# Optimization experiments

Measured on AMD Instinct MI355X. Metric: run time of the kernel, lower is better.

The kernel has to match this reference:

```python
import jax, jax.numpy as jnp
import numpy as np

N_NODES = 100000
N_EDGES = 3200000
D = 256
REPEAT = 2
FACTOR = 0.5


def setup_inputs() -> dict:
    key = jax.random.key(0)
    k1, k2, k3, k4, k5, k6 = jax.random.split(key, 6)
    x = jax.random.normal(k1, (N_NODES, D), dtype=jnp.float32)
    vals = jax.random.uniform(k2, (N_EDGES,), dtype=jnp.float32)
    # Xavier-ish scale for linear weights
    W0 = jax.random.normal(k3, (D, D), dtype=jnp.float32) / np.sqrt(D)
    W1 = jax.random.normal(k4, (D, D), dtype=jnp.float32) / np.sqrt(D)
    rows = jax.random.randint(k5, (N_EDGES,), 0, N_NODES, dtype=jnp.int32)
    cols = jax.random.randint(k6, (N_EDGES,), 0, N_NODES, dtype=jnp.int32)
    return {"x": x, "vals": vals, "W0": W0, "W1": W1, "rows": rows, "cols": cols}


def reference(x, vals, W0, W1, rows, cols):
    # support is sparse [N, N] in COO: support[rows[e], cols[e]] = vals[e]
    def spmm(h):
        # gather source-node features, scale by edge weight, scatter-add to dst
        return jax.ops.segment_sum(vals[:, None] * h[cols], rows,
                                   num_segments=N_NODES)

    h = x
    for W, act in ((W0, jax.nn.relu), (W1, lambda v: v)):
        # _propagate: repeated SpMM with scalar factor
        for _ in range(REPEAT):
            h = spmm(h) * FACTOR
        # linear (no bias) + activation
        h = act(h @ W)
    return h
```

## Files before the change

### kernel.cpp

```cpp
#include <hip/hip_runtime.h>
#include <hip/hip_bf16.h>
#include <hip/hip_fp16.h>

#define N_D 256
#define NBLK 832

typedef __attribute__((ext_vector_type(8))) short bf16x8;
typedef __attribute__((ext_vector_type(4))) float f32x4;

__device__ __forceinline__ unsigned short f2bf(float f) {
  union { float f; unsigned u; } c; c.f = f;
  unsigned u = c.u;
  return (unsigned short)((u + 0x7fffu + ((u >> 16) & 1u)) >> 16);
}
__device__ __forceinline__ float asf(unsigned u) {
  union { unsigned u; float f; } c; c.u = u;
  return c.f;
}
__device__ __forceinline__ int grp_of(int r, unsigned gmagic) {
  int g = (int)(((unsigned long long)(unsigned)r * gmagic) >> 37);
  return min(g, 7);
}

__global__ __launch_bounds__(256) void conv_kernel(
    const float* __restrict__ in, unsigned short* __restrict__ out, int n4) {
  int i = blockIdx.x * 256 + threadIdx.x;
  if (i < n4) {
    float4 v = reinterpret_cast<const float4*>(in)[i];
    ushort4 o;
    o.x = f2bf(v.x); o.y = f2bf(v.y); o.z = f2bf(v.z); o.w = f2bf(v.w);
    reinterpret_cast<ushort4*>(out)[i] = o;
  }
}

__global__ __launch_bounds__(256) void count_kernel(
    const int* __restrict__ rows, int* __restrict__ cnt8, int* __restrict__ cntT,
    int n_edges, unsigned gmagic, int M) {
  __shared__ int lcnt[8];
  if (threadIdx.x < 8) lcnt[threadIdx.x] = 0;
  __syncthreads();
  int* __restrict__ cnt = cnt8 + (size_t)(blockIdx.x & 7) * M;
  for (int e = blockIdx.x * 256 + threadIdx.x; e < n_edges; e += NBLK * 256) {
    const int r = rows[e];
    atomicAdd(&cnt[r], 1);
    atomicAdd(&lcnt[grp_of(r, gmagic)], 1);
  }
  __syncthreads();
  if (threadIdx.x < 8) cntT[threadIdx.x * NBLK + blockIdx.x] = lcnt[threadIdx.x];
}

__global__ __launch_bounds__(256) void sumcnt_kernel(
    const int* __restrict__ cnt8, int* __restrict__ cnts,
    int* __restrict__ bsum, int M) {
  __shared__ int wred[4];
  const int i = blockIdx.x * 256 + threadIdx.x;
  int s = 0;
  if (i < M) {
#pragma unroll
    for (int k = 0; k < 8; ++k) s += cnt8[(size_t)k * M + i];
    cnts[i] = s;
  }
  int t = s;
#pragma unroll
  for (int off = 32; off; off >>= 1) t += __shfl_down(t, off, 64);
  if ((threadIdx.x & 63) == 0) wred[threadIdx.x >> 6] = t;
  __syncthreads();
  if (threadIdx.x == 0) bsum[blockIdx.x] = wred[0] + wred[1] + wred[2] + wred[3];
}

__global__ __launch_bounds__(1024) void scan_kernel(
    const int* __restrict__ cnt, int* __restrict__ outA,
    int* __restrict__ outB, int n) {
  __shared__ int wsum[16];
  __shared__ int carry_sh;
  const int tid = threadIdx.x;
  const int lane = tid & 63;
  const int wid = tid >> 6;
  if (tid == 0) carry_sh = 0;
  __syncthreads();
  for (int base = 0; base < n; base += 4096) {
    const int i0 = base + tid * 4;
    int4 v = make_int4(0, 0, 0, 0);
    if (i0 + 3 < n) v = *reinterpret_cast<const int4*>(cnt + i0);
    else {
      if (i0     < n) v.x = cnt[i0];
      if (i0 + 1 < n) v.y = cnt[i0 + 1];
      if (i0 + 2 < n) v.z = cnt[i0 + 2];
    }
    const int s1 = v.x, s2 = s1 + v.y, s3 = s2 + v.z, s4 = s3 + v.w;
    int ws = s4;
#pragma unroll
    for (int off = 1; off < 64; off <<= 1) {
      int o = __shfl_up(ws, off, 64);
      if (lane >= off) ws += o;
    }
    if (lane == 63) wsum[wid] = ws;
    __syncthreads();
    if (wid == 0) {
      int t = (lane < 16) ? wsum[lane] : 0;
#pragma unroll
      for (int off = 1; off < 16; off <<= 1) {
        int o = __shfl_up(t, off, 64);
        if (lane >= off) t += o;
      }
      if (lane < 16) wsum[lane] = t;
    }
    __syncthreads();
    const int carry = carry_sh;
    const int tbase = carry + (wid ? wsum[wid - 1] : 0) + ws - s4;
    if (i0     < n) { outA[i0]     = tbase;      outB[i0]     = tbase; }
    if (i0 + 1 < n) { outA[i0 + 1] = tbase + s1; outB[i0 + 1] = tbase + s1; }
    if (i0 + 2 < n) { outA[i0 + 2] = tbase + s2; outB[i0 + 2] = tbase + s2; }
    if (i0 + 3 < n) { outA[i0 + 3] = tbase + s3; outB[i0 + 3] = tbase + s3; }
    __syncthreads();
    if (tid == 0) carry_sh = carry + wsum[15];
    __syncthreads();
  }
  if (tid == 0) outA[n] = carry_sh;
}

__global__ __launch_bounds__(256) void scan_apply_kernel(
    const int* __restrict__ cnts, const int* __restrict__ bofs,
    int* __restrict__ row_ptr, int* __restrict__ cursor, int M) {
  __shared__ int wsum[4];
  const int tid = threadIdx.x;
  const int lane = tid & 63;
  const int wid = tid >> 6;
  const int i = blockIdx.x * 256 + tid;
  const int v = (i < M) ? cnts[i] : 0;
  int s = v;
#pragma unroll
  for (int off = 1; off < 64; off <<= 1) {
    int o = __shfl_up(s, off, 64);
    if (lane >= off) s += o;
  }
  if (lane == 63) wsum[wid] = s;
  __syncthreads();
  int add = 0;
  for (int k = 0; k < wid; ++k) add += wsum[k];
  const int excl = bofs[blockIdx.x] + add + s - v;
  if (i < M) { row_ptr[i] = excl; cursor[i] = excl; }
  if (i == M) row_ptr[M] = bofs[gridDim.x];
}

__global__ __launch_bounds__(256) void partition_kernel(
    const int* __restrict__ rows, const int* __restrict__ cols,
    const float* __restrict__ vals, const int* __restrict__ pofsT,
    int2* __restrict__ part, int n_edges, unsigned gmagic) {
  __shared__ int lofs[8];
  if (threadIdx.x < 8) lofs[threadIdx.x] = pofsT[threadIdx.x * NBLK + blockIdx.x];
  __syncthreads();
  for (int e = blockIdx.x * 256 + threadIdx.x; e < n_edges; e += NBLK * 256) {
    const int r = rows[e];
    const int g = grp_of(r, gmagic);
    const int slot = atomicAdd(&lofs[g], 1);
    const unsigned short hb = __half_as_ushort(__float2half_rn(vals[e] * 0.5f));
    int2 rv;
    rv.x = r;
    rv.y = (int)(((unsigned)cols[e] << 15) | ((unsigned)hb >> 1));
    part[slot] = rv;
  }
}

__global__ __launch_bounds__(256) void scatter2_kernel(
    const int2* __restrict__ part, const int* __restrict__ pofsT,
    int* __restrict__ cursor, unsigned* __restrict__ colpack) {
  const int g  = blockIdx.x & 7;
  const int bk = blockIdx.x >> 3;
  const int nb = gridDim.x >> 3;
  const int s0 = pofsT[g * NBLK];
  const int s1 = pofsT[(g + 1) * NBLK];
  for (int i = s0 + bk * 256 + threadIdx.x; i < s1; i += nb * 256) {
    const int2 rv = part[i];
    const int pos = atomicAdd(&cursor[rv.x], 1);
    colpack[pos] = (unsigned)rv.y;
  }
}

__global__ __launch_bounds__(256) void spmm_slice(
    const unsigned short* __restrict__ hin, const int* __restrict__ row_ptr,
    const unsigned* __restrict__ colpack, unsigned short* __restrict__ hout,
    int n_nodes) {
  const int slice = blockIdx.x & 3;
  const int lane = threadIdx.x & 63;
  const int half = lane >> 5;
  const int sub  = lane & 31;
  const int wgid = ((blockIdx.x >> 2) * 256 + threadIdx.x) >> 6;
  const int node = wgid * 2 + half;
  const bool ok = node < n_nodes;
  int start = 0, end = 0;
  if (ok) { start = row_ptr[node]; end = row_ptr[node + 1]; }

  const unsigned* __restrict__ hinw = reinterpret_cast<const unsigned*>(hin);
  const int fofs = slice * 32 + sub;
  const int sbase = half << 5;

  float acc0 = 0.f, acc1 = 0.f;

  for (int base = start; base < end; base += 32) {
    const int cnt = min(32, end - base);
    unsigned u = 0;
    if (base + sub < end) u = colpack[base + sub];
    const int opre = (int)((u >> 15) << 7);
    const float vpre = __half2float(__ushort_as_half((unsigned short)((u & 0x7fffu) << 1)));
    for (int t = 0; t < cnt; t += 8) {
      unsigned hv[8];
      float v[8];
#pragma unroll
      for (int j = 0; j < 8; ++j) {
        const int oj = __shfl(opre, sbase + t + j, 64);
        v[j] = __shfl(vpre, sbase + t + j, 64);
        hv[j] = hinw[(size_t)(unsigned)(oj + fofs)];
      }
#pragma unroll
      for (int j = 0; j < 8; ++j) {
        acc0 += v[j] * asf(hv[j] << 16);
        acc1 += v[j] * asf(hv[j] & 0xffff0000u);
      }
    }
  }
  if (ok) {
    reinterpret_cast<unsigned*>(hout)[(size_t)node * 128 + fofs] =
        (unsigned)f2bf(acc0) | ((unsigned)f2bf(acc1) << 16);
  }
}

__global__ __launch_bounds__(256) void wconv_kernel(
    const float* __restrict__ W, unsigned short* __restrict__ WT) {
  int k = blockIdx.x;
  int n = threadIdx.x;
  WT[(size_t)n * N_D + k] = f2bf(W[(size_t)k * N_D + n]);
}

template <bool RELU, bool OUT_BF16>
__global__ __launch_bounds__(256) void gemm2(
    const unsigned short* __restrict__ H, const unsigned short* __restrict__ WT,
    void* __restrict__ C, int M) {
  const int wave = threadIdx.x >> 6;
  const int lane = threadIdx.x & 63;
  const int m = lane & 15;
  const int p = lane >> 4;
  const int row0 = blockIdx.x * 64 + wave * 16;

  f32x4 acc[16];
#pragma unroll
  for (int i = 0; i < 16; ++i) acc[i] = (f32x4){0.f, 0.f, 0.f, 0.f};

  const int r = row0 + m;
  const bool rok = r < M;

  for (int k0 = 0; k0 < N_D; k0 += 32) {
    bf16x8 a = {0, 0, 0, 0, 0, 0, 0, 0};
    if (rok) a = *reinterpret_cast<const bf16x8*>(H + (size_t)r * N_D + k0 + p * 8);
#pragma unroll
    for (int nt = 0; nt < 16; ++nt) {
      const bf16x8 b = *reinterpret_cast<const bf16x8*>(
          WT + (size_t)(nt * 16 + m) * N_D + k0 + p * 8);
      acc[nt] = __builtin_amdgcn_mfma_f32_16x16x32_bf16(a, b, acc[nt], 0, 0, 0);
    }
  }

#pragma unroll
  for (int nt = 0; nt < 16; ++nt) {
    const int col = nt * 16 + m;
#pragma unroll
    for (int rr = 0; rr < 4; ++rr) {
      const int r2 = row0 + p * 4 + rr;
      if (r2 < M) {
        float vv = acc[nt][rr];
        if (RELU) vv = fmaxf(vv, 0.f);
        if (OUT_BF16)
          ((unsigned short*)C)[(size_t)r2 * N_D + col] = f2bf(vv);
        else
          ((float*)C)[(size_t)r2 * N_D + col] = vv;
      }
    }
  }
}

extern "C" void kernel_launch(void* const* d_in, const int* in_sizes, int n_in,
                              void* d_out, int out_size, void* d_ws, size_t ws_size,
                              hipStream_t stream) {
  const float* x    = (const float*)d_in[0];
  const float* vals = (const float*)d_in[1];
  const float* W0   = (const float*)d_in[2];
  const float* W1   = (const float*)d_in[3];
  const int*   rows = (const int*)d_in[4];
  const int*   cols = (const int*)d_in[5];

  const int n_edges = in_sizes[1];
  const int M = in_sizes[0] / N_D;
  const size_t n_feat = (size_t)M * N_D;

  char* ws = (char*)d_ws;
  unsigned short* hA      = (unsigned short*)(ws);
  unsigned*       colpack = (unsigned*)(ws + 51200000);
  int*            row_ptr = (int*)(ws + 64000000);
  int*            cursor  = (int*)(ws + 64400128);
  int*            cnt8    = (int*)(ws + 64800256);
  int*            cnts    = (int*)(ws + 68000384);
  int*            bsum    = (int*)(ws + 68400512);
  int*            bofs    = (int*)(ws + 68402560);
  int*            bscr    = (int*)(ws + 68404608);
  int*            cntT    = (int*)(ws + 68406656);
  int*            pofsT   = (int*)(ws + 68433536);
  int*            pscr    = (int*)(ws + 68460416);
  unsigned short* wt      = (unsigned short*)(ws + 68487296);
  unsigned short* hB   = (unsigned short*)d_out;
  unsigned short* xb   = (unsigned short*)d_out + n_feat;
  int2*           part = (int2*)((char*)d_out + 51200000);

  const int Mb = (M + 255) / 256;
  const int sblocks = 4 * ((M + 7) / 8);
  const int gblocks = (M + 63) / 64;
  const int cblocks = (int)(n_feat / 4 + 255) / 256;
  const int rpg = (M + 7) / 8;
  const unsigned gmagic = (unsigned)(((1ULL << 37) + rpg - 1) / (unsigned long long)rpg);

  hipMemsetAsync(cnt8, 0, (size_t)8 * M * sizeof(int), stream);
  count_kernel<<<NBLK, 256, 0, stream>>>(rows, cnt8, cntT, n_edges, gmagic, M);
  sumcnt_kernel<<<Mb, 256, 0, stream>>>(cnt8, cnts, bsum, M);
  scan_kernel<<<1, 1024, 0, stream>>>(bsum, bofs, bscr, Mb);
  scan_apply_kernel<<<Mb, 256, 0, stream>>>(cnts, bofs, row_ptr, cursor, M);
  scan_kernel<<<1, 1024, 0, stream>>>(cntT, pofsT, pscr, 8 * NBLK);
  partition_kernel<<<NBLK, 256, 0, stream>>>(rows, cols, vals, pofsT, part,
                                             n_edges, gmagic);
  scatter2_kernel<<<NBLK, 256, 0, stream>>>(part, pofsT, cursor, colpack);
  conv_kernel<<<cblocks, 256, 0, stream>>>(x, xb, (int)(n_feat / 4));

  spmm_slice<<<sblocks, 256, 0, stream>>>(xb, row_ptr, colpack, hA, M);
  spmm_slice<<<sblocks, 256, 0, stream>>>(hA, row_ptr, colpack, hB, M);
  wconv_kernel<<<N_D, N_D, 0, stream>>>(W0, wt);
  gemm2<true, true><<<gblocks, 256, 0, stream>>>(hB, wt, hA, M);

  spmm_slice<<<sblocks, 256, 0, stream>>>(hA, row_ptr, colpack, hB, M);
  spmm_slice<<<sblocks, 256, 0, stream>>>(hB, row_ptr, colpack, hA, M);
  wconv_kernel<<<N_D, N_D, 0, stream>>>(W1, wt);
  gemm2<false, false><<<gblocks, 256, 0, stream>>>(hA, wt, d_out, M);
}
```

Measured before the change: 1.273 ms.

## Apply linear before propagation, fuse relu/f32 output into SpMM, drop conversion kernel

Measured after the change: 1.290 ms. Within noise of the previous version (+1.3%).

```diff
diff --git a/kernel.cpp b/kernel.cpp
--- a/kernel.cpp
+++ b/kernel.cpp
@@ -7,6 +7,8 @@
 
 typedef __attribute__((ext_vector_type(8))) short bf16x8;
 typedef __attribute__((ext_vector_type(4))) float f32x4;
+typedef __attribute__((ext_vector_type(2))) float f32x2;
+typedef __attribute__((ext_vector_type(2))) int   i32x2;
 
 __device__ __forceinline__ unsigned short f2bf(float f) {
   union { float f; unsigned u; } c; c.f = f;
@@ -20,17 +22,6 @@
 __device__ __forceinline__ int grp_of(int r, unsigned gmagic) {
   int g = (int)(((unsigned long long)(unsigned)r * gmagic) >> 37);
   return min(g, 7);
-}
-
-__global__ __launch_bounds__(256) void conv_kernel(
-    const float* __restrict__ in, unsigned short* __restrict__ out, int n4) {
-  int i = blockIdx.x * 256 + threadIdx.x;
-  if (i < n4) {
-    float4 v = reinterpret_cast<const float4*>(in)[i];
-    ushort4 o;
-    o.x = f2bf(v.x); o.y = f2bf(v.y); o.z = f2bf(v.z); o.w = f2bf(v.w);
-    reinterpret_cast<ushort4*>(out)[i] = o;
-  }
 }
 
 __global__ __launch_bounds__(256) void count_kernel(
@@ -41,7 +32,7 @@
   __syncthreads();
   int* __restrict__ cnt = cnt8 + (size_t)(blockIdx.x & 7) * M;
   for (int e = blockIdx.x * 256 + threadIdx.x; e < n_edges; e += NBLK * 256) {
-    const int r = rows[e];
+    const int r = __builtin_nontemporal_load(&rows[e]);
     atomicAdd(&cnt[r], 1);
     atomicAdd(&lcnt[grp_of(r, gmagic)], 1);
   }
@@ -146,24 +137,26 @@
 __global__ __launch_bounds__(256) void partition_kernel(
     const int* __restrict__ rows, const int* __restrict__ cols,
     const float* __restrict__ vals, const int* __restrict__ pofsT,
-    int2* __restrict__ part, int n_edges, unsigned gmagic) {
+    i32x2* __restrict__ part, int n_edges, unsigned gmagic) {
   __shared__ int lofs[8];
   if (threadIdx.x < 8) lofs[threadIdx.x] = pofsT[threadIdx.x * NBLK + blockIdx.x];
   __syncthreads();
   for (int e = blockIdx.x * 256 + threadIdx.x; e < n_edges; e += NBLK * 256) {
-    const int r = rows[e];
+    const int r = __builtin_nontemporal_load(&rows[e]);
+    const int c = __builtin_nontemporal_load(&cols[e]);
+    const float vl = __builtin_nontemporal_load(&vals[e]);
     const int g = grp_of(r, gmagic);
     const int slot = atomicAdd(&lofs[g], 1);
-    const unsigned short hb = __half_as_ushort(__float2half_rn(vals[e] * 0.5f));
-    int2 rv;
+    const unsigned short hb = __half_as_ushort(__float2half_rn(vl * 0.5f));
+    i32x2 rv;
     rv.x = r;
-    rv.y = (int)(((unsigned)cols[e] << 15) | ((unsigned)hb >> 1));
-    part[slot] = rv;
+    rv.y = (int)(((unsigned)c << 15) | ((unsigned)hb >> 1));
+    __builtin_nontemporal_store(rv, &part[slot]);
   }
 }
 
 __global__ __launch_bounds__(256) void scatter2_kernel(
-    const int2* __restrict__ part, const int* __restrict__ pofsT,
+    const i32x2* __restrict__ part, const int* __restrict__ pofsT,
     int* __restrict__ cursor, unsigned* __restrict__ colpack) {
   const int g  = blockIdx.x & 7;
   const int bk = blockIdx.x >> 3;
@@ -171,15 +164,16 @@
   const int s0 = pofsT[g * NBLK];
   const int s1 = pofsT[(g + 1) * NBLK];
   for (int i = s0 + bk * 256 + threadIdx.x; i < s1; i += nb * 256) {
-    const int2 rv = part[i];
+    const i32x2 rv = __builtin_nontemporal_load(&part[i]);
     const int pos = atomicAdd(&cursor[rv.x], 1);
     colpack[pos] = (unsigned)rv.y;
   }
 }
 
+template <bool RELU, bool F32OUT>
 __global__ __launch_bounds__(256) void spmm_slice(
     const unsigned short* __restrict__ hin, const int* __restrict__ row_ptr,
-    const unsigned* __restrict__ colpack, unsigned short* __restrict__ hout,
+    const unsigned* __restrict__ colpack, void* __restrict__ hout,
     int n_nodes) {
   const int slice = blockIdx.x & 3;
   const int lane = threadIdx.x & 63;
@@ -200,42 +194,51 @@
   for (int base = start; base < end; base += 32) {
     const int cnt = min(32, end - base);
     unsigned u = 0;
-    if (base + sub < end) u = colpack[base + sub];
-    const int opre = (int)((u >> 15) << 7);
-    const float vpre = __half2float(__ushort_as_half((unsigned short)((u & 0x7fffu) << 1)));
-    for (int t = 0; t < cnt; t += 8) {
-      unsigned hv[8];
-      float v[8];
-#pragma unroll
-      for (int j = 0; j < 8; ++j) {
-        const int oj = __shfl(opre, sbase + t + j, 64);
-        v[j] = __shfl(vpre, sbase + t + j, 64);
-        hv[j] = hinw[(size_t)(unsigned)(oj + fofs)];
-      }
-#pragma unroll
-      for (int j = 0; j < 8; ++j) {
+    if (base + sub < end) u = __builtin_nontemporal_load(&colpack[base + sub]);
+    for (int t = 0; t < cnt; t += 16) {
+      unsigned hv[16];
+      float v[16];
+#pragma unroll
+      for (int j = 0; j < 16; ++j) {
+        const unsigned ue = (unsigned)__shfl((int)u, sbase + t + j, 64);
+        const int c = (int)(ue >> 15);
+        v[j] = __half2float(__ushort_as_half((unsigned short)((ue & 0x7fffu) << 1)));
+        hv[j] = hinw[(size_t)c * 128 + fofs];
+      }
+#pragma unroll
+      for (int j = 0; j < 16; ++j) {
         acc0 += v[j] * asf(hv[j] << 16);
         acc1 += v[j] * asf(hv[j] & 0xffff0000u);
       }
     }
   }
   if (ok) {
-    reinterpret_cast<unsigned*>(hout)[(size_t)node * 128 + fofs] =
-        (unsigned)f2bf(acc0) | ((unsigned)f2bf(acc1) << 16);
+    if (RELU) { acc0 = fmaxf(acc0, 0.f); acc1 = fmaxf(acc1, 0.f); }
+    if (F32OUT) {
+      f32x2 o; o.x = acc0; o.y = acc1;
+      __builtin_nontemporal_store(o, reinterpret_cast<f32x2*>(hout) + (size_t)node * 128 + fofs);
+    } else {
+      unsigned o = (unsigned)f2bf(acc0) | ((unsigned)f2bf(acc1) << 16);
+      __builtin_nontemporal_store(o, reinterpret_cast<unsigned*>(hout) + (size_t)node * 128 + fofs);
+    }
   }
 }
 
 __global__ __launch_bounds__(256) void wconv_kernel(
-    const float* __restrict__ W, unsigned short* __restrict__ WT) {
-  int k = blockIdx.x;
-  int n = threadIdx.x;
+    const float* __restrict__ W0, const float* __restrict__ W1,
+    unsigned short* __restrict__ WT0, unsigned short* __restrict__ WT1) {
+  const int w = blockIdx.x >> 8;
+  const int k = blockIdx.x & 255;
+  const int n = threadIdx.x;
+  const float* W = w ? W1 : W0;
+  unsigned short* WT = w ? WT1 : WT0;
   WT[(size_t)n * N_D + k] = f2bf(W[(size_t)k * N_D + n]);
 }
 
-template <bool RELU, bool OUT_BF16>
+template <bool AF32>
 __global__ __launch_bounds__(256) void gemm2(
-    const unsigned short* __restrict__ H, const unsigned short* __restrict__ WT,
-    void* __restrict__ C, int M) {
+    const void* __restrict__ H, const unsigned short* __restrict__ WT,
+    unsigned short* __restrict__ C, int M) {
   const int wave = threadIdx.x >> 6;
   const int lane = threadIdx.x & 63;
   const int m = lane & 15;
@@ -251,7 +254,18 @@
 
   for (int k0 = 0; k0 < N_D; k0 += 32) {
     bf16x8 a = {0, 0, 0, 0, 0, 0, 0, 0};
-    if (rok) a = *reinterpret_cast<const bf16x8*>(H + (size_t)r * N_D + k0 + p * 8);
+    if (rok) {
+      if (AF32) {
+        const float* ap = (const float*)H + (size_t)r * N_D + k0 + p * 8;
+        const float4 f0 = *reinterpret_cast<const float4*>(ap);
+        const float4 f1 = *reinterpret_cast<const float4*>(ap + 4);
+        a[0] = f2bf(f0.x); a[1] = f2bf(f0.y); a[2] = f2bf(f0.z); a[3] = f2bf(f0.w);
+        a[4] = f2bf(f1.x); a[5] = f2bf(f1.y); a[6] = f2bf(f1.z); a[7] = f2bf(f1.w);
+      } else {
+        a = *reinterpret_cast<const bf16x8*>(
+            (const unsigned short*)H + (size_t)r * N_D + k0 + p * 8);
+      }
+    }
 #pragma unroll
     for (int nt = 0; nt < 16; ++nt) {
       const bf16x8 b = *reinterpret_cast<const bf16x8*>(
@@ -267,12 +281,7 @@
     for (int rr = 0; rr < 4; ++rr) {
       const int r2 = row0 + p * 4 + rr;
       if (r2 < M) {
-        float vv = acc[nt][rr];
-        if (RELU) vv = fmaxf(vv, 0.f);
-        if (OUT_BF16)
-          ((unsigned short*)C)[(size_t)r2 * N_D + col] = f2bf(vv);
-        else
-          ((float*)C)[(size_t)r2 * N_D + col] = vv;
+        C[(size_t)r2 * N_D + col] = f2bf(acc[nt][rr]);
       }
     }
   }
@@ -305,15 +314,15 @@
   int*            cntT    = (int*)(ws + 68406656);
   int*            pofsT   = (int*)(ws + 68433536);
   int*            pscr    = (int*)(ws + 68460416);
-  unsigned short* wt      = (unsigned short*)(ws + 68487296);
+  unsigned short* wt0     = (unsigned short*)(ws + 68487296);
+  unsigned short* wt1     = (unsigned short*)(ws + 68618368);
   unsigned short* hB   = (unsigned short*)d_out;
-  unsigned short* xb   = (unsigned short*)d_out + n_feat;
-  int2*           part = (int2*)((char*)d_out + 51200000);
+  unsigned short* hC   = (unsigned short*)d_out + n_feat;
+  i32x2*          part = (i32x2*)((char*)d_out + 51200000);
 
   const int Mb = (M + 255) / 256;
   const int sblocks = 4 * ((M + 7) / 8);
   const int gblocks = (M + 63) / 64;
-  const int cblocks = (int)(n_feat / 4 + 255) / 256;
   const int rpg = (M + 7) / 8;
   const unsigned gmagic = (unsigned)(((1ULL << 37) + rpg - 1) / (unsigned long long)rpg);
 
@@ -326,15 +335,13 @@
   partition_kernel<<<NBLK, 256, 0, stream>>>(rows, cols, vals, pofsT, part,
                                              n_edges, gmagic);
   scatter2_kernel<<<NBLK, 256, 0, stream>>>(part, pofsT, cursor, colpack);
-  conv_kernel<<<cblocks, 256, 0, stream>>>(x, xb, (int)(n_feat / 4));
-
-  spmm_slice<<<sblocks, 256, 0, stream>>>(xb, row_ptr, colpack, hA, M);
-  spmm_slice<<<sblocks, 256, 0, stream>>>(hA, row_ptr, colpack, hB, M);
-  wconv_kernel<<<N_D, N_D, 0, stream>>>(W0, wt);
-  gemm2<true, true><<<gblocks, 256, 0, stream>>>(hB, wt, hA, M);
-
-  spmm_slice<<<sblocks, 256, 0, stream>>>(hA, row_ptr, colpack, hB, M);
-  spmm_slice<<<sblocks, 256, 0, stream>>>(hB, row_ptr, colpack, hA, M);
-  wconv_kernel<<<N_D, N_D, 0, stream>>>(W1, wt);
-  gemm2<false, false><<<gblocks, 256, 0, stream>>>(hA, wt, d_out, M);
-}
+  wconv_kernel<<<512, 256, 0, stream>>>(W0, W1, wt0, wt1);
+
+  gemm2<true ><<<gblocks, 256, 0, stream>>>(x,  wt0, hB, M);
+  spmm_slice<false, false><<<sblocks, 256, 0, stream>>>(hB, row_ptr, colpack, hA, M);
+  spmm_slice<true,  false><<<sblocks, 256, 0, stream>>>(hA, row_ptr, colpack, hB, M);
+
+  gemm2<false><<<gblocks, 256, 0, stream>>>(hB, wt1, hC, M);
+  spmm_slice<false, false><<<sblocks, 256, 0, stream>>>(hC, row_ptr, colpack, hA, M);
+  spmm_slice<false, true ><<<sblocks, 256, 0, stream>>>(hA, row_ptr, colpack, d_out, M);
+}
```
